# Kernel optimization log

Measured on AMD Instinct MI355X. Metric: run time of the kernel, lower is better.

Reference implementation:

```python
import jax, jax.numpy as jnp
import numpy as np

B, S, D = 4, 4096, 128

def setup_inputs() -> dict:
    key = jax.random.key(0)
    kx, kq, kk, kv = jax.random.split(key, 4)
    x = jax.random.normal(kx, (B, S, D), dtype=jnp.float32)
    Wq = jax.random.normal(kq, (D, D), dtype=jnp.float32) * (1.0 / np.sqrt(D))
    Wk = jax.random.normal(kk, (D, D), dtype=jnp.float32) * (1.0 / np.sqrt(D))
    Wv = jax.random.normal(kv, (D, D), dtype=jnp.float32) * (1.0 / np.sqrt(D))
    return {"x": x, "Wq": Wq, "Wk": Wk, "Wv": Wv}

def reference(x, Wq, Wk, Wv):
    b, s, d = x.shape
    # nn.Linear(bias=False): y = x @ W.T
    q = jnp.einsum('bsd,ed->bse', x, Wq)
    k = jnp.einsum('bsd,ed->bse', x, Wk)
    v = jnp.einsum('bsd,ed->bse', x, Wv)
    scores = jnp.einsum('bqd,bkd->bqk', q, k) / jnp.sqrt(jnp.float32(d))
    causal = jnp.tril(jnp.ones((s, s), dtype=bool))  # [s,s]
    scores = jnp.where(causal, scores, jnp.float32(-jnp.inf))
    weights = jax.nn.softmax(scores.astype(jnp.float32), axis=-1)
    out = jnp.einsum('bqk,bkd->bqd', weights, v)
    return out  # dropout is identity in eval / p=0
```

## Files before the change

### kernel.cpp

```cpp
#include <hip/hip_runtime.h>
#include <hip/hip_bf16.h>
#include <math.h>

typedef __attribute__((ext_vector_type(8))) short short8;
typedef __attribute__((ext_vector_type(4))) float f32x4;
typedef __attribute__((ext_vector_type(4))) float float4v;
typedef __attribute__((ext_vector_type(4))) unsigned short ushort4v;

typedef __attribute__((address_space(1))) const unsigned int GAS;
typedef __attribute__((address_space(3))) unsigned int LAS;

#define B_ 4
#define S_ 4096
#define D_ 128

#define CPB 544
#define NSLOT (B_ * CPB)

#define LDS_K 0
#define LDS_V 16384
#define LDS_P 32768
#define LDS_TOTAL 40960

__device__ __forceinline__ unsigned short f2bf(float f) {
    union { float f; unsigned u; } v; v.f = f;
    unsigned r = v.u + 0x7FFFu + ((v.u >> 16) & 1u);
    return (unsigned short)(r >> 16);
}
__device__ __forceinline__ float bf2f(unsigned short h) {
    union { unsigned u; float f; } v; v.u = ((unsigned)h) << 16;
    return v.f;
}

__global__ void wconv_kernel(const float* __restrict__ Wq,
                             const float* __restrict__ Wk,
                             const float* __restrict__ Wv,
                             unsigned short* __restrict__ Wb) {
    int i = blockIdx.x * 256 + threadIdx.x;
    if (i >= 3 * 16384) return;
    const float* s = (i < 16384) ? Wq : (i < 32768 ? Wk : Wv);
    Wb[i] = f2bf(s[i & 16383]);
}

__global__ __launch_bounds__(256) void qkv_kernel(const float* __restrict__ X,
                                                  const unsigned short* __restrict__ Wb,
                                                  unsigned short* __restrict__ Qb,
                                                  unsigned short* __restrict__ Kb,
                                                  unsigned short* __restrict__ Vt) {
    const int tid = threadIdx.x;
    const int lane = tid & 63, w = tid >> 6;
    const int l16 = lane & 15, g = lane >> 4;
    const int r0 = blockIdx.x * 64;
    const int grp = blockIdx.y;

    const int row = r0 + w * 16 + l16;
    const float* xr = X + (long)row * 128;
    float4v x0[4], x1[4];
    #pragma unroll
    for (int kb = 0; kb < 4; ++kb) {
        x0[kb] = *reinterpret_cast<const float4v*>(xr + kb * 32 + g * 8);
        x1[kb] = *reinterpret_cast<const float4v*>(xr + kb * 32 + g * 8 + 4);
    }
    short8 a[4];
    #pragma unroll
    for (int kb = 0; kb < 4; ++kb) {
        short8 t;
        t[0] = f2bf(x0[kb][0]); t[1] = f2bf(x0[kb][1]);
        t[2] = f2bf(x0[kb][2]); t[3] = f2bf(x0[kb][3]);
        t[4] = f2bf(x1[kb][0]); t[5] = f2bf(x1[kb][1]);
        t[6] = f2bf(x1[kb][2]); t[7] = f2bf(x1[kb][3]);
        a[kb] = t;
    }

    #pragma unroll
    for (int ct = 0; ct < 8; ++ct) {
        const int e = ct * 16 + l16;
        const int c = grp * 128 + e;
        f32x4 acc = {0.f, 0.f, 0.f, 0.f};
        #pragma unroll
        for (int kb = 0; kb < 4; ++kb) {
            short8 bf = *reinterpret_cast<const short8*>(Wb + (long)c * 128 + kb * 32 + g * 8);
            acc = __builtin_amdgcn_mfma_f32_16x16x32_bf16(a[kb], bf, acc, 0, 0, 0);
        }
        const int row0 = r0 + w * 16 + g * 4;
        if (grp == 0) {
            #pragma unroll
            for (int r = 0; r < 4; ++r) Qb[(long)(row0 + r) * 128 + e] = f2bf(acc[r]);
        } else if (grp == 1) {
            #pragma unroll
            for (int r = 0; r < 4; ++r) Kb[(long)(row0 + r) * 128 + e] = f2bf(acc[r]);
        } else {
            const int bb = row0 >> 12, ss = row0 & 4095;
            ushort4v p;
            p[0] = f2bf(acc[0]); p[1] = f2bf(acc[1]); p[2] = f2bf(acc[2]); p[3] = f2bf(acc[3]);
            *reinterpret_cast<ushort4v*>(&Vt[((long)bb * 128 + e) * 4096 + ss]) = p;
        }
    }
}

__global__ __launch_bounds__(256) void attn_kernel(const unsigned short* __restrict__ Qb,
                                                   const unsigned short* __restrict__ Kb,
                                                   const unsigned short* __restrict__ Vt,
                                                   unsigned short* __restrict__ Opart,
                                                   float* __restrict__ Mpart,
                                                   float* __restrict__ Lpart) {
    __shared__ __align__(16) unsigned char lds[LDS_TOTAL];

    const int tid = threadIdx.x;
    const int lane = tid & 63, w = tid >> 6;
    const int l16 = lane & 15, g = lane >> 4;

    const int bidx = (int)blockIdx.x;
    const int b = bidx / CPB;
    const int rr = CPB - 1 - (bidx - b * CPB);
    int gg = 0;
    while (2 * (gg + 1) * (gg + 2) <= rr) ++gg;
    const int j = rr - 2 * gg * (gg + 1);
    const int qt = 4 * gg + j / (gg + 1);
    const int c = j % (gg + 1);
    const int slot = b * CPB + rr;

    const unsigned short* Qbase = Qb + (long)b * S_ * D_;
    const unsigned char* Kb_b = (const unsigned char*)(Kb + (long)b * S_ * D_);
    const unsigned char* Vb_b = (const unsigned char*)(Vt + (long)b * D_ * S_);

    const int qrow_f = qt * 64 + w * 16 + l16;
    short8 qf[4];
    #pragma unroll
    for (int kb = 0; kb < 4; ++kb)
        qf[kb] = *reinterpret_cast<const short8*>(Qbase + (long)qrow_f * 128 + kb * 32 + g * 8);

    int koff[4], voff[4];
    #pragma unroll
    for (int i = 0; i < 4; ++i) {
        int ch = w * 4 + i;
        int krow = ch * 4 + g;
        koff[i] = krow * 256 + ((l16 * 16) ^ ((krow & 7) << 4));
        int vrow = ch * 8 + (lane >> 3);
        voff[i] = vrow * 8192 + (((lane & 7) * 16) ^ ((vrow & 7) << 4));
    }

    f32x4 o[8];
    #pragma unroll
    for (int dt = 0; dt < 8; ++dt) o[dt] = (f32x4){0.f, 0.f, 0.f, 0.f};
    float m[4], lsum[4];
    int myrow[4];
    #pragma unroll
    for (int r = 0; r < 4; ++r) {
        m[r] = -INFINITY; lsum[r] = 0.f;
        myrow[r] = qt * 64 + w * 16 + g * 4 + r;
    }

    const float scale = 0.08838834764831845f;
    const int kt0 = c * 4;
    const int ktend = min(kt0 + 3, qt);

    unsigned char* Pw = lds + LDS_P + w * 2048;

    for (int kt = kt0; kt <= ktend; ++kt) {
        #pragma unroll
        for (int i = 0; i < 4; ++i) {
            int ch = w * 4 + i;
            __builtin_amdgcn_global_load_lds((GAS*)(Kb_b + (long)kt * 16384 + koff[i]),
                                             (LAS*)(lds + LDS_K + ch * 1024), 16, 0, 0);
            __builtin_amdgcn_global_load_lds((GAS*)(Vb_b + (long)kt * 128 + voff[i]),
                                             (LAS*)(lds + LDS_V + ch * 1024), 16, 0, 0);
        }
        __syncthreads();

        f32x4 s[4];
        __builtin_amdgcn_s_setprio(1);
        #pragma unroll
        for (int ct = 0; ct < 4; ++ct) {
            s[ct] = (f32x4){0.f, 0.f, 0.f, 0.f};
            const int kvl = ct * 16 + l16;
            #pragma unroll
            for (int kb = 0; kb < 4; ++kb) {
                int byt = (kvl * 256 + kb * 64 + g * 16) ^ ((kvl & 7) << 4);
                short8 kf = *reinterpret_cast<const short8*>(lds + byt);
                s[ct] = __builtin_amdgcn_mfma_f32_16x16x32_bf16(qf[kb], kf, s[ct], 0, 0, 0);
            }
        }
        __builtin_amdgcn_s_setprio(0);

        const bool diag = (kt == qt);
        float rmax[4] = {-1e30f, -1e30f, -1e30f, -1e30f};
        #pragma unroll
        for (int ct = 0; ct < 4; ++ct) {
            #pragma unroll
            for (int r = 0; r < 4; ++r) {
                float sv = s[ct][r] * scale;
                if (diag && (kt * 64 + ct * 16 + l16 > myrow[r])) sv = -1e30f;
                s[ct][r] = sv;
                rmax[r] = fmaxf(rmax[r], sv);
            }
        }
        #pragma unroll
        for (int off = 1; off < 16; off <<= 1) {
            #pragma unroll
            for (int r = 0; r < 4; ++r) rmax[r] = fmaxf(rmax[r], __shfl_xor(rmax[r], off, 64));
        }
        bool upd = false;
        #pragma unroll
        for (int r = 0; r < 4; ++r) upd = upd || (rmax[r] > m[r] + 8.0f);
        if (__any(upd)) {
            float al[4];
            #pragma unroll
            for (int r = 0; r < 4; ++r) {
                float mn = fmaxf(m[r], rmax[r]);
                al[r] = __expf(m[r] - mn);
                m[r] = mn;
                lsum[r] *= al[r];
            }
            #pragma unroll
            for (int dt = 0; dt < 8; ++dt) {
                #pragma unroll
                for (int r = 0; r < 4; ++r) o[dt][r] *= al[r];
            }
        }
        float rsum[4] = {0.f, 0.f, 0.f, 0.f};
        #pragma unroll
        for (int ct = 0; ct < 4; ++ct) {
            #pragma unroll
            for (int r = 0; r < 4; ++r) {
                float p = __expf(s[ct][r] - m[r]);
                s[ct][r] = p;
                rsum[r] += p;
            }
        }
        #pragma unroll
        for (int off = 1; off < 16; off <<= 1) {
            #pragma unroll
            for (int r = 0; r < 4; ++r) rsum[r] += __shfl_xor(rsum[r], off, 64);
        }
        #pragma unroll
        for (int r = 0; r < 4; ++r) lsum[r] += rsum[r];

        #pragma unroll
        for (int ct = 0; ct < 4; ++ct) {
            #pragma unroll
            for (int r = 0; r < 4; ++r) {
                int pr = g * 4 + r, pc = ct * 16 + l16;
                int byt = (pr * 128 + pc * 2) ^ ((pr & 7) << 4);
                *reinterpret_cast<unsigned short*>(Pw + byt) = f2bf(s[ct][r]);
            }
        }

        #pragma unroll
        for (int kvb = 0; kvb < 2; ++kvb) {
            int pbyt = (l16 * 128 + kvb * 64 + g * 16) ^ ((l16 & 7) << 4);
            short8 pf = *reinterpret_cast<const short8*>(Pw + pbyt);
            __builtin_amdgcn_s_setprio(1);
            #pragma unroll
            for (int dt = 0; dt < 8; ++dt) {
                int d = dt * 16 + l16;
                int vbyt = LDS_V + ((d * 128 + kvb * 64 + g * 16) ^ ((d & 7) << 4));
                short8 vf = *reinterpret_cast<const short8*>(lds + vbyt);
                o[dt] = __builtin_amdgcn_mfma_f32_16x16x32_bf16(pf, vf, o[dt], 0, 0, 0);
            }
            __builtin_amdgcn_s_setprio(0);
        }

        if (kt < ktend) __syncthreads();
    }

    unsigned short* Op = Opart + (long)slot * 8192;
    #pragma unroll
    for (int dt = 0; dt < 8; ++dt) {
        #pragma unroll
        for (int r = 0; r < 4; ++r) {
            Op[(w * 16 + g * 4 + r) * 128 + dt * 16 + l16] = f2bf(o[dt][r]);
        }
    }
    if (l16 == 0) {
        #pragma unroll
        for (int r = 0; r < 4; ++r) {
            Mpart[(long)slot * 64 + w * 16 + g * 4 + r] = m[r];
            Lpart[(long)slot * 64 + w * 16 + g * 4 + r] = lsum[r];
        }
    }
}

__global__ __launch_bounds__(256) void combine_kernel(const unsigned short* __restrict__ Opart,
                                                      const float* __restrict__ Mpart,
                                                      const float* __restrict__ Lpart,
                                                      float* __restrict__ out) {
    __shared__ float coeff[16][16];
    __shared__ float invL[16];

    const int qt = blockIdx.x >> 2, qq = blockIdx.x & 3, b = blockIdx.y;
    const int gg = qt >> 2;
    const int nc = gg + 1;
    const int slot0 = b * CPB + 2 * gg * (gg + 1) + (qt - 4 * gg) * nc;
    const int r0 = qq * 16;

    const int tid = threadIdx.x;
    if (tid < 16) {
        float mg = -INFINITY;
        for (int c = 0; c < nc; ++c)
            mg = fmaxf(mg, Mpart[(long)(slot0 + c) * 64 + r0 + tid]);
        float L = 0.f;
        for (int c = 0; c < nc; ++c) {
            float co = __expf(Mpart[(long)(slot0 + c) * 64 + r0 + tid] - mg);
            coeff[c][tid] = co;
            L += co * Lpart[(long)(slot0 + c) * 64 + r0 + tid];
        }
        invL[tid] = 1.f / L;
    }
    __syncthreads();

    const int e0 = tid * 8;
    const int r = e0 >> 7;
    float acc[8];
    #pragma unroll
    for (int k = 0; k < 8; ++k) acc[k] = 0.f;
    for (int c = 0; c < nc; ++c) {
        short8 v = *reinterpret_cast<const short8*>(Opart + (long)(slot0 + c) * 8192 + r0 * 128 + e0);
        const float co = coeff[c][r];
        #pragma unroll
        for (int k = 0; k < 8; ++k)
            acc[k] += co * bf2f((unsigned short)v[k]);
    }
    const float s = invL[r];
    float4v o0, o1;
    o0[0] = acc[0] * s; o0[1] = acc[1] * s; o0[2] = acc[2] * s; o0[3] = acc[3] * s;
    o1[0] = acc[4] * s; o1[1] = acc[5] * s; o1[2] = acc[6] * s; o1[3] = acc[7] * s;
    float* dst = out + ((long)b * S_ + qt * 64 + r0) * 128 + e0;
    *reinterpret_cast<float4v*>(dst) = o0;
    *reinterpret_cast<float4v*>(dst + 4) = o1;
}

extern "C" void kernel_launch(void* const* d_in, const int* in_sizes, int n_in,
                              void* d_out, int out_size, void* d_ws, size_t ws_size,
                              hipStream_t stream) {
    (void)in_sizes; (void)n_in; (void)out_size; (void)ws_size;
    const float* x  = (const float*)d_in[0];
    const float* Wq = (const float*)d_in[1];
    const float* Wk = (const float*)d_in[2];
    const float* Wv = (const float*)d_in[3];
    float* out = (float*)d_out;

    char* ws = (char*)d_ws;
    const size_t MB4 = (size_t)16384 * 128 * 2;
    unsigned short* Qb = (unsigned short*)(ws);
    unsigned short* Kb = (unsigned short*)(ws + MB4);
    unsigned short* Vt = (unsigned short*)(ws + 2 * MB4);
    unsigned short* Wb = (unsigned short*)(ws + 3 * MB4);
    unsigned short* Opart = (unsigned short*)(ws + 3 * MB4 + (1 << 20));
    float* Mpart = (float*)(ws + 3 * MB4 + (1 << 20) + (size_t)NSLOT * 8192 * 2);
    float* Lpart = Mpart + (size_t)NSLOT * 64;

    wconv_kernel<<<192, 256, 0, stream>>>(Wq, Wk, Wv, Wb);
    qkv_kernel<<<dim3(256, 3), 256, 0, stream>>>(x, Wb, Qb, Kb, Vt);
    attn_kernel<<<NSLOT, 256, 0, stream>>>(Qb, Kb, Vt, Opart, Mpart, Lpart);
    combine_kernel<<<dim3(256, 4), 256, 0, stream>>>(Opart, Mpart, Lpart, out);
}
```

Baseline: 154.8 us.

## Use 128-row query tiles with 8 waves and double-buffered V prefetch

The attention kernel now processes 128 query rows per block with 512 threads, so each loaded K/V tile is shared by twice as many waves and the number of split-K slots is halved. The next K/V tile is prefetched into LDS while softmax and PV run, with V double-buffered and K reloaded after the QK barrier. The softmax scale is folded into Q during the projection, removing a multiply per score. This costs more LDS per block (64KB), which may reduce occupancy, and it changes the partial-sum layout used by the combine kernel.

```diff
diff --git a/kernel.cpp b/kernel.cpp
--- a/kernel.cpp
+++ b/kernel.cpp
@@ -14,13 +14,13 @@
 #define S_ 4096
 #define D_ 128
 
-#define CPB 544
+#define CPB 272
 #define NSLOT (B_ * CPB)
 
 #define LDS_K 0
 #define LDS_V 16384
-#define LDS_P 32768
-#define LDS_TOTAL 40960
+#define LDS_P 49152
+#define LDS_TOTAL 65536
 
 __device__ __forceinline__ unsigned short f2bf(float f) {
     union { float f; unsigned u; } v; v.f = f;
@@ -72,6 +72,7 @@
         a[kb] = t;
     }
 
+    const float scale = 0.08838834764831845f;
     #pragma unroll
     for (int ct = 0; ct < 8; ++ct) {
         const int e = ct * 16 + l16;
@@ -85,7 +86,7 @@
         const int row0 = r0 + w * 16 + g * 4;
         if (grp == 0) {
             #pragma unroll
-            for (int r = 0; r < 4; ++r) Qb[(long)(row0 + r) * 128 + e] = f2bf(acc[r]);
+            for (int r = 0; r < 4; ++r) Qb[(long)(row0 + r) * 128 + e] = f2bf(acc[r] * scale);
         } else if (grp == 1) {
             #pragma unroll
             for (int r = 0; r < 4; ++r) Kb[(long)(row0 + r) * 128 + e] = f2bf(acc[r]);
@@ -98,7 +99,7 @@
     }
 }
 
-__global__ __launch_bounds__(256) void attn_kernel(const unsigned short* __restrict__ Qb,
+__global__ __launch_bounds__(512) void attn_kernel(const unsigned short* __restrict__ Qb,
                                                    const unsigned short* __restrict__ Kb,
                                                    const unsigned short* __restrict__ Vt,
                                                    unsigned short* __restrict__ Opart,
@@ -112,32 +113,34 @@
 
     const int bidx = (int)blockIdx.x;
     const int b = bidx / CPB;
-    const int rr = CPB - 1 - (bidx - b * CPB);
-    int gg = 0;
-    while (2 * (gg + 1) * (gg + 2) <= rr) ++gg;
-    const int j = rr - 2 * gg * (gg + 1);
-    const int qt = 4 * gg + j / (gg + 1);
-    const int c = j % (gg + 1);
-    const int slot = b * CPB + rr;
+    const int rr = bidx - b * CPB;
+    int h = 0;
+    while ((h + 1) * (h + 2) <= rr) ++h;
+    int qt, c;
+    {
+        int rem = rr - h * (h + 1);
+        if (rem < h + 1) { qt = 2 * h; c = rem; }
+        else             { qt = 2 * h + 1; c = rr - (h + 1) * (h + 1); }
+    }
+    const int slot = bidx;
 
     const unsigned short* Qbase = Qb + (long)b * S_ * D_;
     const unsigned char* Kb_b = (const unsigned char*)(Kb + (long)b * S_ * D_);
     const unsigned char* Vb_b = (const unsigned char*)(Vt + (long)b * D_ * S_);
 
-    const int qrow_f = qt * 64 + w * 16 + l16;
+    const int qrow_f = qt * 128 + w * 16 + l16;
     short8 qf[4];
     #pragma unroll
     for (int kb = 0; kb < 4; ++kb)
         qf[kb] = *reinterpret_cast<const short8*>(Qbase + (long)qrow_f * 128 + kb * 32 + g * 8);
 
-    int koff[4], voff[4];
-    #pragma unroll
-    for (int i = 0; i < 4; ++i) {
-        int ch = w * 4 + i;
-        int krow = ch * 4 + g;
-        koff[i] = krow * 256 + ((l16 * 16) ^ ((krow & 7) << 4));
-        int vrow = ch * 8 + (lane >> 3);
-        voff[i] = vrow * 8192 + (((lane & 7) * 16) ^ ((vrow & 7) << 4));
+    int koff[2], voff[2];
+    #pragma unroll
+    for (int it = 0; it < 2; ++it) {
+        int krow = it * 32 + w * 4 + (lane >> 4);
+        koff[it] = krow * 256 + ((l16 * 16) ^ ((krow & 7) << 4));
+        int vrow = it * 64 + w * 8 + (lane >> 3);
+        voff[it] = vrow * 8192 + (((lane & 7) * 16) ^ ((vrow & 7) << 4));
     }
 
     f32x4 o[8];
@@ -148,25 +151,29 @@
     #pragma unroll
     for (int r = 0; r < 4; ++r) {
         m[r] = -INFINITY; lsum[r] = 0.f;
-        myrow[r] = qt * 64 + w * 16 + g * 4 + r;
-    }
-
-    const float scale = 0.08838834764831845f;
+        myrow[r] = qt * 128 + w * 16 + g * 4 + r;
+    }
+
     const int kt0 = c * 4;
-    const int ktend = min(kt0 + 3, qt);
+    const int ktend = min(kt0 + 3, 2 * qt + 1);
 
     unsigned char* Pw = lds + LDS_P + w * 2048;
 
+    {
+        const int buf0 = kt0 & 1;
+        #pragma unroll
+        for (int it = 0; it < 2; ++it) {
+            __builtin_amdgcn_global_load_lds((GAS*)(Kb_b + (long)kt0 * 16384 + koff[it]),
+                                             (LAS*)(lds + LDS_K + it * 8192 + w * 1024), 16, 0, 0);
+            __builtin_amdgcn_global_load_lds((GAS*)(Vb_b + (long)kt0 * 128 + voff[it]),
+                                             (LAS*)(lds + LDS_V + buf0 * 16384 + it * 8192 + w * 1024), 16, 0, 0);
+        }
+    }
+    __syncthreads();
+
     for (int kt = kt0; kt <= ktend; ++kt) {
-        #pragma unroll
-        for (int i = 0; i < 4; ++i) {
-            int ch = w * 4 + i;
-            __builtin_amdgcn_global_load_lds((GAS*)(Kb_b + (long)kt * 16384 + koff[i]),
-                                             (LAS*)(lds + LDS_K + ch * 1024), 16, 0, 0);
-            __builtin_amdgcn_global_load_lds((GAS*)(Vb_b + (long)kt * 128 + voff[i]),
-                                             (LAS*)(lds + LDS_V + ch * 1024), 16, 0, 0);
-        }
-        __syncthreads();
+        const int buf = kt & 1;
+        const bool more = (kt < ktend);
 
         f32x4 s[4];
         __builtin_amdgcn_s_setprio(1);
@@ -183,14 +190,26 @@
         }
         __builtin_amdgcn_s_setprio(0);
 
-        const bool diag = (kt == qt);
+        __syncthreads();
+
+        if (more) {
+            #pragma unroll
+            for (int it = 0; it < 2; ++it) {
+                __builtin_amdgcn_global_load_lds((GAS*)(Kb_b + (long)(kt + 1) * 16384 + koff[it]),
+                                                 (LAS*)(lds + LDS_K + it * 8192 + w * 1024), 16, 0, 0);
+                __builtin_amdgcn_global_load_lds((GAS*)(Vb_b + (long)(kt + 1) * 128 + voff[it]),
+                                                 (LAS*)(lds + LDS_V + (buf ^ 1) * 16384 + it * 8192 + w * 1024), 16, 0, 0);
+            }
+        }
+
+        const bool anymask = (kt * 64 + 63 > qt * 128 + w * 16);
         float rmax[4] = {-1e30f, -1e30f, -1e30f, -1e30f};
         #pragma unroll
         for (int ct = 0; ct < 4; ++ct) {
             #pragma unroll
             for (int r = 0; r < 4; ++r) {
-                float sv = s[ct][r] * scale;
-                if (diag && (kt * 64 + ct * 16 + l16 > myrow[r])) sv = -1e30f;
+                float sv = s[ct][r];
+                if (anymask && (kt * 64 + ct * 16 + l16 > myrow[r])) sv = -1e30f;
                 s[ct][r] = sv;
                 rmax[r] = fmaxf(rmax[r], sv);
             }
@@ -254,17 +273,17 @@
             #pragma unroll
             for (int dt = 0; dt < 8; ++dt) {
                 int d = dt * 16 + l16;
-                int vbyt = LDS_V + ((d * 128 + kvb * 64 + g * 16) ^ ((d & 7) << 4));
+                int vbyt = LDS_V + buf * 16384 + ((d * 128 + kvb * 64 + g * 16) ^ ((d & 7) << 4));
                 short8 vf = *reinterpret_cast<const short8*>(lds + vbyt);
                 o[dt] = __builtin_amdgcn_mfma_f32_16x16x32_bf16(pf, vf, o[dt], 0, 0, 0);
             }
             __builtin_amdgcn_s_setprio(0);
         }
 
-        if (kt < ktend) __syncthreads();
-    }
-
-    unsigned short* Op = Opart + (long)slot * 8192;
+        if (more) __syncthreads();
+    }
+
+    unsigned short* Op = Opart + (long)slot * 16384;
     #pragma unroll
     for (int dt = 0; dt < 8; ++dt) {
         #pragma unroll
@@ -275,8 +294,8 @@
     if (l16 == 0) {
         #pragma unroll
         for (int r = 0; r < 4; ++r) {
-            Mpart[(long)slot * 64 + w * 16 + g * 4 + r] = m[r];
-            Lpart[(long)slot * 64 + w * 16 + g * 4 + r] = lsum[r];
+            Mpart[(long)slot * 128 + w * 16 + g * 4 + r] = m[r];
+            Lpart[(long)slot * 128 + w * 16 + g * 4 + r] = lsum[r];
         }
     }
 }
@@ -288,22 +307,23 @@
     __shared__ float coeff[16][16];
     __shared__ float invL[16];
 
-    const int qt = blockIdx.x >> 2, qq = blockIdx.x & 3, b = blockIdx.y;
-    const int gg = qt >> 2;
-    const int nc = gg + 1;
-    const int slot0 = b * CPB + 2 * gg * (gg + 1) + (qt - 4 * gg) * nc;
+    const int qt = blockIdx.x >> 3, qq = blockIdx.x & 7, b = blockIdx.y;
+    const int h = qt >> 1;
+    const int nc = h + 1;
+    const int sbase = (qt & 1) ? (h + 1) * (h + 1) : h * (h + 1);
+    const int slot0 = b * CPB + sbase;
     const int r0 = qq * 16;
 
     const int tid = threadIdx.x;
     if (tid < 16) {
         float mg = -INFINITY;
         for (int c = 0; c < nc; ++c)
-            mg = fmaxf(mg, Mpart[(long)(slot0 + c) * 64 + r0 + tid]);
+            mg = fmaxf(mg, Mpart[(long)(slot0 + c) * 128 + r0 + tid]);
         float L = 0.f;
         for (int c = 0; c < nc; ++c) {
-            float co = __expf(Mpart[(long)(slot0 + c) * 64 + r0 + tid] - mg);
+            float co = __expf(Mpart[(long)(slot0 + c) * 128 + r0 + tid] - mg);
             coeff[c][tid] = co;
-            L += co * Lpart[(long)(slot0 + c) * 64 + r0 + tid];
+            L += co * Lpart[(long)(slot0 + c) * 128 + r0 + tid];
         }
         invL[tid] = 1.f / L;
     }
@@ -315,7 +335,7 @@
     #pragma unroll
     for (int k = 0; k < 8; ++k) acc[k] = 0.f;
     for (int c = 0; c < nc; ++c) {
-        short8 v = *reinterpret_cast<const short8*>(Opart + (long)(slot0 + c) * 8192 + r0 * 128 + e0);
+        short8 v = *reinterpret_cast<const short8*>(Opart + (long)(slot0 + c) * 16384 + r0 * 128 + e0);
         const float co = coeff[c][r];
         #pragma unroll
         for (int k = 0; k < 8; ++k)
@@ -325,7 +345,7 @@
     float4v o0, o1;
     o0[0] = acc[0] * s; o0[1] = acc[1] * s; o0[2] = acc[2] * s; o0[3] = acc[3] * s;
     o1[0] = acc[4] * s; o1[1] = acc[5] * s; o1[2] = acc[6] * s; o1[3] = acc[7] * s;
-    float* dst = out + ((long)b * S_ + qt * 64 + r0) * 128 + e0;
+    float* dst = out + ((long)b * S_ + qt * 128 + r0) * 128 + e0;
     *reinterpret_cast<float4v*>(dst) = o0;
     *reinterpret_cast<float4v*>(dst + 4) = o1;
 }
@@ -347,11 +367,11 @@
     unsigned short* Vt = (unsigned short*)(ws + 2 * MB4);
     unsigned short* Wb = (unsigned short*)(ws + 3 * MB4);
     unsigned short* Opart = (unsigned short*)(ws + 3 * MB4 + (1 << 20));
-    float* Mpart = (float*)(ws + 3 * MB4 + (1 << 20) + (size_t)NSLOT * 8192 * 2);
-    float* Lpart = Mpart + (size_t)NSLOT * 64;
+    float* Mpart = (float*)(ws + 3 * MB4 + (1 << 20) + (size_t)NSLOT * 16384 * 2);
+    float* Lpart = Mpart + (size_t)NSLOT * 128;
 
     wconv_kernel<<<192, 256, 0, stream>>>(Wq, Wk, Wv, Wb);
     qkv_kernel<<<dim3(256, 3), 256, 0, stream>>>(x, Wb, Qb, Kb, Vt);
-    attn_kernel<<<NSLOT, 256, 0, stream>>>(Qb, Kb, Vt, Opart, Mpart, Lpart);
+    attn_kernel<<<NSLOT, 512, 0, stream>>>(Qb, Kb, Vt, Opart, Mpart, Lpart);
     combine_kernel<<<dim3(256, 4), 256, 0, stream>>>(Opart, Mpart, Lpart, out);
 }
```

After: 155.7 us. No clear change (+0.6%).

## Fold softmax scale into Q projection, precompute LDS addresses, set occupancy hint

Applied to the files above, without the earlier changes.

The softmax scale is applied when Q is written in the projection kernel, which removes a per-score multiply in the attention loop. K/V chunk loads are reindexed so consecutive threads write consecutive 16-byte LDS slots. LDS read and write addresses for K, V and P are precomputed outside the loop so the inner MFMA loops use constant offsets. Causal masking now runs only on the diagonal tile, and launch_bounds(256,4) asks for higher occupancy, at the risk of register pressure or spills and a small change in rounding from scaling before the bf16 conversion.

```diff
diff --git a/kernel.cpp b/kernel.cpp
--- a/kernel.cpp
+++ b/kernel.cpp
@@ -72,6 +72,7 @@
         a[kb] = t;
     }
 
+    const float scale = 0.08838834764831845f;
     #pragma unroll
     for (int ct = 0; ct < 8; ++ct) {
         const int e = ct * 16 + l16;
@@ -85,7 +86,7 @@
         const int row0 = r0 + w * 16 + g * 4;
         if (grp == 0) {
             #pragma unroll
-            for (int r = 0; r < 4; ++r) Qb[(long)(row0 + r) * 128 + e] = f2bf(acc[r]);
+            for (int r = 0; r < 4; ++r) Qb[(long)(row0 + r) * 128 + e] = f2bf(acc[r] * scale);
         } else if (grp == 1) {
             #pragma unroll
             for (int r = 0; r < 4; ++r) Kb[(long)(row0 + r) * 128 + e] = f2bf(acc[r]);
@@ -98,12 +99,12 @@
     }
 }
 
-__global__ __launch_bounds__(256) void attn_kernel(const unsigned short* __restrict__ Qb,
-                                                   const unsigned short* __restrict__ Kb,
-                                                   const unsigned short* __restrict__ Vt,
-                                                   unsigned short* __restrict__ Opart,
-                                                   float* __restrict__ Mpart,
-                                                   float* __restrict__ Lpart) {
+__global__ __launch_bounds__(256, 4) void attn_kernel(const unsigned short* __restrict__ Qb,
+                                                      const unsigned short* __restrict__ Kb,
+                                                      const unsigned short* __restrict__ Vt,
+                                                      unsigned short* __restrict__ Opart,
+                                                      float* __restrict__ Mpart,
+                                                      float* __restrict__ Lpart) {
     __shared__ __align__(16) unsigned char lds[LDS_TOTAL];
 
     const int tid = threadIdx.x;
@@ -133,12 +134,36 @@
     int koff[4], voff[4];
     #pragma unroll
     for (int i = 0; i < 4; ++i) {
-        int ch = w * 4 + i;
-        int krow = ch * 4 + g;
-        koff[i] = krow * 256 + ((l16 * 16) ^ ((krow & 7) << 4));
-        int vrow = ch * 8 + (lane >> 3);
-        voff[i] = vrow * 8192 + (((lane & 7) * 16) ^ ((vrow & 7) << 4));
-    }
+        int ch = i * 256 + tid;
+        int krow = ch >> 4, kcd = ch & 15;
+        koff[i] = krow * 256 + ((kcd * 16) ^ ((krow & 7) << 4));
+        int vrow = ch >> 3, vck = ch & 7;
+        voff[i] = vrow * 8192 + ((vck * 16) ^ ((vrow & 7) << 4));
+    }
+
+    const int swz = (l16 & 7) << 4;
+    const unsigned char* kaddr[4];
+    const unsigned char* vaddr[2];
+    const unsigned char* pread[2];
+    unsigned char* Pw = lds + LDS_P + w * 2048;
+    #pragma unroll
+    for (int i = 0; i < 4; ++i)
+        kaddr[i] = lds + LDS_K + l16 * 256 + ((i * 64 + g * 16) ^ swz);
+    #pragma unroll
+    for (int i = 0; i < 2; ++i) {
+        const int xo = (i * 64 + g * 16) ^ swz;
+        vaddr[i] = lds + LDS_V + l16 * 128 + xo;
+        pread[i] = Pw + l16 * 128 + xo;
+    }
+    unsigned char* prow[4];
+    int pmask[4];
+    #pragma unroll
+    for (int r = 0; r < 4; ++r) {
+        const int pr = g * 4 + r;
+        prow[r] = Pw + pr * 128;
+        pmask[r] = (pr & 7) << 4;
+    }
+    const int pl2 = l16 * 2;
 
     f32x4 o[8];
     #pragma unroll
@@ -151,20 +176,17 @@
         myrow[r] = qt * 64 + w * 16 + g * 4 + r;
     }
 
-    const float scale = 0.08838834764831845f;
     const int kt0 = c * 4;
     const int ktend = min(kt0 + 3, qt);
 
-    unsigned char* Pw = lds + LDS_P + w * 2048;
-
     for (int kt = kt0; kt <= ktend; ++kt) {
         #pragma unroll
         for (int i = 0; i < 4; ++i) {
-            int ch = w * 4 + i;
+            int ch = i * 256 + tid;
             __builtin_amdgcn_global_load_lds((GAS*)(Kb_b + (long)kt * 16384 + koff[i]),
-                                             (LAS*)(lds + LDS_K + ch * 1024), 16, 0, 0);
+                                             (LAS*)(lds + LDS_K + ch * 16), 16, 0, 0);
             __builtin_amdgcn_global_load_lds((GAS*)(Vb_b + (long)kt * 128 + voff[i]),
-                                             (LAS*)(lds + LDS_V + ch * 1024), 16, 0, 0);
+                                             (LAS*)(lds + LDS_V + ch * 16), 16, 0, 0);
         }
         __syncthreads();
 
@@ -173,28 +195,28 @@
         #pragma unroll
         for (int ct = 0; ct < 4; ++ct) {
             s[ct] = (f32x4){0.f, 0.f, 0.f, 0.f};
-            const int kvl = ct * 16 + l16;
             #pragma unroll
             for (int kb = 0; kb < 4; ++kb) {
-                int byt = (kvl * 256 + kb * 64 + g * 16) ^ ((kvl & 7) << 4);
-                short8 kf = *reinterpret_cast<const short8*>(lds + byt);
+                short8 kf = *reinterpret_cast<const short8*>(kaddr[kb] + ct * 4096);
                 s[ct] = __builtin_amdgcn_mfma_f32_16x16x32_bf16(qf[kb], kf, s[ct], 0, 0, 0);
             }
         }
         __builtin_amdgcn_s_setprio(0);
 
-        const bool diag = (kt == qt);
-        float rmax[4] = {-1e30f, -1e30f, -1e30f, -1e30f};
-        #pragma unroll
-        for (int ct = 0; ct < 4; ++ct) {
-            #pragma unroll
-            for (int r = 0; r < 4; ++r) {
-                float sv = s[ct][r] * scale;
-                if (diag && (kt * 64 + ct * 16 + l16 > myrow[r])) sv = -1e30f;
-                s[ct][r] = sv;
-                rmax[r] = fmaxf(rmax[r], sv);
-            }
-        }
+        if (kt == qt) {
+            #pragma unroll
+            for (int ct = 0; ct < 4; ++ct) {
+                const int col = kt * 64 + ct * 16 + l16;
+                #pragma unroll
+                for (int r = 0; r < 4; ++r)
+                    if (col > myrow[r]) s[ct][r] = -1e30f;
+            }
+        }
+
+        float rmax[4];
+        #pragma unroll
+        for (int r = 0; r < 4; ++r)
+            rmax[r] = fmaxf(fmaxf(s[0][r], s[1][r]), fmaxf(s[2][r], s[3][r]));
         #pragma unroll
         for (int off = 1; off < 16; off <<= 1) {
             #pragma unroll
@@ -240,22 +262,18 @@
         for (int ct = 0; ct < 4; ++ct) {
             #pragma unroll
             for (int r = 0; r < 4; ++r) {
-                int pr = g * 4 + r, pc = ct * 16 + l16;
-                int byt = (pr * 128 + pc * 2) ^ ((pr & 7) << 4);
-                *reinterpret_cast<unsigned short*>(Pw + byt) = f2bf(s[ct][r]);
+                *reinterpret_cast<unsigned short*>(prow[r] + ((ct * 32 + pl2) ^ pmask[r])) =
+                    f2bf(s[ct][r]);
             }
         }
 
         #pragma unroll
         for (int kvb = 0; kvb < 2; ++kvb) {
-            int pbyt = (l16 * 128 + kvb * 64 + g * 16) ^ ((l16 & 7) << 4);
-            short8 pf = *reinterpret_cast<const short8*>(Pw + pbyt);
+            short8 pf = *reinterpret_cast<const short8*>(pread[kvb]);
             __builtin_amdgcn_s_setprio(1);
             #pragma unroll
             for (int dt = 0; dt < 8; ++dt) {
-                int d = dt * 16 + l16;
-                int vbyt = LDS_V + ((d * 128 + kvb * 64 + g * 16) ^ ((d & 7) << 4));
-                short8 vf = *reinterpret_cast<const short8*>(lds + vbyt);
+                short8 vf = *reinterpret_cast<const short8*>(vaddr[kvb] + dt * 2048);
                 o[dt] = __builtin_amdgcn_mfma_f32_16x16x32_bf16(pf, vf, o[dt], 0, 0, 0);
             }
             __builtin_amdgcn_s_setprio(0);
```

New measurement: 141.4 us. 1.09x faster.
